# Kernel tuning notes

Measured on AMD Instinct MI355X. Metric: run time of the kernel, lower is better.

Reference implementation:

```python
import jax, jax.numpy as jnp
import numpy as np

HIDDEN = 1024
N_ROUTED = 16
N_SHARED = 2
TOP_K = 2
MID_R = HIDDEN // 4   # routed_ratio=4 -> 256
MID_S = HIDDEN // 2   # shared_ratio=2 -> 512


def setup_inputs() -> dict:
    key = jax.random.key(0)
    ks = jax.random.split(key, 8)
    s = 0.02
    return {
        "x": jax.random.normal(ks[0], (2, 1024, HIDDEN), dtype=jnp.float32),
        "router_w": jax.random.normal(ks[1], (HIDDEN, N_ROUTED), dtype=jnp.float32) * s,
        "wg_r": jax.random.normal(ks[2], (N_ROUTED, HIDDEN, MID_R), dtype=jnp.float32) * s,
        "wu_r": jax.random.normal(ks[3], (N_ROUTED, HIDDEN, MID_R), dtype=jnp.float32) * s,
        "wd_r": jax.random.normal(ks[4], (N_ROUTED, MID_R, HIDDEN), dtype=jnp.float32) * s,
        "wg_s": jax.random.normal(ks[5], (N_SHARED, HIDDEN, MID_S), dtype=jnp.float32) * s,
        "wu_s": jax.random.normal(ks[6], (N_SHARED, HIDDEN, MID_S), dtype=jnp.float32) * s,
        "wd_s": jax.random.normal(ks[7], (N_SHARED, MID_S, HIDDEN), dtype=jnp.float32) * s,
    }


def reference(x, router_w, wg_r, wu_r, wd_r, wg_s, wu_s, wd_s):
    orig_shape = x.shape
    flat = x.reshape(-1, orig_shape[-1])  # [T, D]

    # ---- shared experts: sum of always-active SwiGLU FFNs ----
    gs = jnp.einsum("td,ndm->tnm", flat, wg_s)            # [T, Ns, Ms]
    us = jnp.einsum("td,ndm->tnm", flat, wu_s)
    out = jnp.einsum("tnm,nmd->td", jax.nn.silu(gs) * us, wd_s)  # summed over n

    # ---- router: softmax -> top-k -> renormalize ----
    logits = (flat @ router_w).astype(jnp.float32)        # [T, E]
    probs = jax.nn.softmax(logits, axis=-1)
    weights, indices = jax.lax.top_k(probs, TOP_K)        # [T, K]
    weights = weights / (weights.sum(axis=-1, keepdims=True) + 1e-9)
    weights = weights.astype(x.dtype)

    # combine weights as dense [T, E] (top-k indices are distinct)
    comb = jnp.sum(jax.nn.one_hot(indices, N_ROUTED, dtype=x.dtype)
                   * weights[..., None], axis=1)          # [T, E]

    # ---- routed experts (dense dispatch; combine folded into hidden) ----
    g = jnp.einsum("td,edm->tem", flat, wg_r)             # [T, E, Mr]
    u = jnp.einsum("td,edm->tem", flat, wu_r)
    h = jax.nn.silu(g) * u                                 # [T, E, Mr]
    h = h * comb[:, :, None]                               # weight before down-proj (linear)
    out = out + jnp.einsum("tem,emd->td", h, wd_r)

    return out.reshape(orig_shape)
```

## Files before the change

kernel.cpp:

```cpp
#include <hip/hip_runtime.h>
#include <hip/hip_bf16.h>
#include <stdint.h>

#define T_TOK 2048
#define DHID  1024
#define NEXP  16
#define MR    256
#define MS    512
#define CAP   512

typedef float  f32x4  __attribute__((ext_vector_type(4)));
typedef __bf16 bf16x8 __attribute__((ext_vector_type(8)));

typedef __attribute__((address_space(3))) void       lds_void;
typedef const __attribute__((address_space(1))) void gbl_void;

#define GLOAD16(g, l) __builtin_amdgcn_global_load_lds((gbl_void*)(g), (lds_void*)(l), 16, 0, 0)
#define VMCNT8() asm volatile("s_waitcnt vmcnt(8)" ::: "memory")
#define VMCNT0() asm volatile("s_waitcnt vmcnt(0)" ::: "memory")
#define SCHED_FENCE() __builtin_amdgcn_sched_barrier(0)

__device__ __forceinline__ void barrier_raw() {
  asm volatile("" ::: "memory");
  __builtin_amdgcn_s_barrier();
  asm volatile("" ::: "memory");
}

__device__ __forceinline__ ushort f2bf(float f) {
  uint32_t u = __float_as_uint(f);
  u = (u + 0x7fffu + ((u >> 16) & 1u)) >> 16;
  return (ushort)u;
}
__device__ __forceinline__ float bf2f(ushort v) { return __uint_as_float(((uint32_t)v) << 16); }

__device__ __forceinline__ void stage128(const ushort* __restrict__ g0, int strideE,
                                         ushort* lds, int tid) {
  const int wave = tid >> 6;
  const int r = tid >> 3, colE = (tid & 7) * 8;
#pragma unroll
  for (int s = 0; s < 4; ++s) {
    const int row = s * 32 + r;
    GLOAD16(g0 + (size_t)row * strideE + (colE ^ ((row & 7) << 3)), lds + s * 2048 + wave * 512);
  }
}

__device__ __forceinline__ void stage_gather128(const ushort* __restrict__ xb,
                                                const int tok[4], int k0,
                                                ushort* lds, int tid) {
  const int wave = tid >> 6;
  const int r = tid >> 3, colE = (tid & 7) * 8;
#pragma unroll
  for (int s = 0; s < 4; ++s) {
    const int row = s * 32 + r;
    GLOAD16(xb + (size_t)tok[s] * DHID + k0 + (colE ^ ((row & 7) << 3)), lds + s * 2048 + wave * 512);
  }
}

__device__ __forceinline__ void mfma_tile(const ushort* a_sh, const ushort* b_sh,
                                          int wr, int wc, int lane, f32x4 (&acc)[4][4]) {
  const int rb = lane & 15;
  const int sw = (rb & 7) << 3;
#pragma unroll
  for (int kk = 0; kk < 64; kk += 32) {
    const int k8 = (kk + ((lane >> 4) << 3)) ^ sw;
    bf16x8 af[4];
#pragma unroll
    for (int m = 0; m < 4; m++)
      af[m] = *(const bf16x8*)&a_sh[(wr * 64 + m * 16 + rb) * 64 + k8];
#pragma unroll
    for (int n = 0; n < 4; n++) {
      bf16x8 bf = *(const bf16x8*)&b_sh[(wc * 64 + n * 16 + rb) * 64 + k8];
#pragma unroll
      for (int m = 0; m < 4; m++)
        acc[m][n] = __builtin_amdgcn_mfma_f32_16x16x32_bf16(af[m], bf, acc[m][n], 0, 0, 0);
    }
  }
}

__device__ __forceinline__ bool queue_lookup(const int* __restrict__ cnt, int mti,
                                             int& e_out, int& s0_out, int& c_out) {
  int acc = 0;
#pragma unroll
  for (int ee = 0; ee < NEXP; ++ee) {
    const int c = cnt[ee];
    const int ntl = (c + 127) >> 7;
    if (mti < acc + ntl) { e_out = ee; s0_out = (mti - acc) << 7; c_out = c; return true; }
    acc += ntl;
  }
  return false;
}

struct TP {
  const float* in; ushort* out;
  int R, C, out_ld, ilv;
  long long out_batch;
};

__device__ __forceinline__ void tpose_tile(const TP p, int local, void* smem, int tid) {
  float (*t_sh)[65] = (float(*)[65])smem;
  const int tr = p.R >> 6, tc = p.C >> 6, per = tr * tc;
  const int b = local / per, rem = local - b * per;
  const int rt = rem / tc, ct = rem - rt * tc;
  const int r0 = rt * 64, c0 = ct * 64;
  const float* ip = p.in + (size_t)b * p.R * p.C;
  ushort* op = p.out + (size_t)b * p.out_batch;
  const int trd = tid >> 4, tcd = (tid & 15) * 4;
#pragma unroll
  for (int q = 0; q < 4; q++) {
    float4 v = *(const float4*)&ip[(size_t)(r0 + trd + q * 16) * p.C + c0 + tcd];
    t_sh[trd + q * 16][tcd + 0] = v.x; t_sh[trd + q * 16][tcd + 1] = v.y;
    t_sh[trd + q * 16][tcd + 2] = v.z; t_sh[trd + q * 16][tcd + 3] = v.w;
  }
  __syncthreads();
#pragma unroll
  for (int q = 0; q < 4; q++) {
    const int cc = trd + q * 16;
    int rr = c0 + cc;
    if (p.ilv) rr = ((rr >> 4) << 5) + (rr & 15);
    ushort4 o;
    o.x = f2bf(t_sh[tcd + 0][cc]); o.y = f2bf(t_sh[tcd + 1][cc]);
    o.z = f2bf(t_sh[tcd + 2][cc]); o.w = f2bf(t_sh[tcd + 3][cc]);
    *(ushort4*)&op[(size_t)rr * p.out_ld + r0 + tcd] = o;
  }
}

__global__ __launch_bounds__(256) void k_prep(
    const float* __restrict__ x, const float* __restrict__ rw,
    ushort* __restrict__ xb, int* __restrict__ topi, float2* __restrict__ topw)
{
  __shared__ float rw_sh[NEXP][DHID];
  const int tid = threadIdx.x;
#pragma unroll
  for (int it = 0; it < 16; ++it) {
    const int flat = it * 1024 + tid * 4;
    float4 v = *(const float4*)&rw[flat];
    const int d = flat >> 4, e = flat & 15;
    rw_sh[e + 0][d] = v.x; rw_sh[e + 1][d] = v.y;
    rw_sh[e + 2][d] = v.z; rw_sh[e + 3][d] = v.w;
  }
  __syncthreads();

  const int wave = tid >> 6, lane = tid & 63;
  for (int tk = 0; tk < 2; ++tk) {
    const int t = blockIdx.x * 8 + wave * 2 + tk;
    const float* xp = x + (size_t)t * DHID;
    float acc[NEXP];
#pragma unroll
    for (int e = 0; e < NEXP; e++) acc[e] = 0.f;
#pragma unroll
    for (int i = 0; i < 4; ++i) {
      const int d4 = i * 64 + lane;
      float4 xv = *(const float4*)&xp[d4 * 4];
      ushort4 o; o.x = f2bf(xv.x); o.y = f2bf(xv.y); o.z = f2bf(xv.z); o.w = f2bf(xv.w);
      *(ushort4*)&xb[(size_t)t * DHID + d4 * 4] = o;
#pragma unroll
      for (int e = 0; e < NEXP; e++) {
        float4 wv = *(const float4*)&rw_sh[e][d4 * 4];
        acc[e] = fmaf(xv.x, wv.x, acc[e]);
        acc[e] = fmaf(xv.y, wv.y, acc[e]);
        acc[e] = fmaf(xv.z, wv.z, acc[e]);
        acc[e] = fmaf(xv.w, wv.w, acc[e]);
      }
    }
#pragma unroll
    for (int off = 32; off >= 1; off >>= 1) {
#pragma unroll
      for (int e = 0; e < NEXP; e++) acc[e] += __shfl_xor(acc[e], off, 64);
    }
    if (lane == 0) {
      float m = acc[0];
#pragma unroll
      for (int e = 1; e < NEXP; e++) m = fmaxf(m, acc[e]);
      float p[NEXP], Z = 0.f;
#pragma unroll
      for (int e = 0; e < NEXP; e++) { p[e] = __expf(acc[e] - m); Z += p[e]; }
      const float inv = 1.f / Z;
      int i1 = 0; float p1 = p[0] * inv;
      for (int e = 1; e < NEXP; e++) { float pe = p[e] * inv; if (pe > p1) { p1 = pe; i1 = e; } }
      int i2 = -1; float p2 = -1.f;
      for (int e = 0; e < NEXP; e++) { if (e == i1) continue; float pe = p[e] * inv; if (pe > p2) { p2 = pe; i2 = e; } }
      const float denom = p1 + p2 + 1e-9f;
      topi[t] = i1 | (i2 << 8);
      topw[t] = make_float2(p1 / denom, p2 / denom);
    }
  }
}

__global__ __launch_bounds__(256) void k_build_tp(
    const int* __restrict__ topi, const float2* __restrict__ topw,
    int* __restrict__ cnt, int* __restrict__ ltok, float* __restrict__ lw,
    int* __restrict__ tslot, TP t0, TP t1, TP t2, TP t3)
{
  __shared__ float t_smem[64][65];
  const int tid = threadIdx.x;
  const int bid = blockIdx.x;
  if (bid >= NEXP) {
    const int local = bid - NEXP;
    if      (local < 1024) tpose_tile(t0, local,        t_smem, tid);
    else if (local < 2048) tpose_tile(t1, local - 1024, t_smem, tid);
    else if (local < 2304) tpose_tile(t2, local - 2048, t_smem, tid);
    else                   tpose_tile(t3, local - 2304, t_smem, tid);
    return;
  }
  int* wsum = (int*)t_smem;
  const int e = bid;
  const int wave = tid >> 6, lane = tid & 63;
  const int t0i = tid * 8;

  int4 a = *(const int4*)&topi[t0i];
  int4 b = *(const int4*)&topi[t0i + 4];
  int ti[8] = {a.x, a.y, a.z, a.w, b.x, b.y, b.z, b.w};
  int match[8]; int c = 0;
#pragma unroll
  for (int k = 0; k < 8; ++k) {
    const int i1 = ti[k] & 0xff, i2 = (ti[k] >> 8) & 0xff;
    match[k] = (i1 == e) ? 1 : ((i2 == e) ? 2 : 0);
    c += (match[k] != 0);
  }
  int incl = c;
#pragma unroll
  for (int off = 1; off < 64; off <<= 1) {
    int n = __shfl_up(incl, off, 64);
    if (lane >= off) incl += n;
  }
  if (lane == 63) wsum[wave] = incl;
  __syncthreads();
  int base = incl - c;
  for (int w = 0; w < wave; ++w) base += wsum[w];
  if (tid == 0) {
    int tot = wsum[0] + wsum[1] + wsum[2] + wsum[3];
    cnt[e] = tot > CAP ? CAP : tot;
  }
#pragma unroll
  for (int k = 0; k < 8; ++k) {
    if (match[k]) {
      const int t = t0i + k;
      if (base < CAP) {
        float2 w2 = topw[t];
        ltok[e * CAP + base] = t;
        lw[e * CAP + base] = (match[k] == 1) ? w2.x : w2.y;
        tslot[t * 2 + (match[k] - 1)] = e * CAP + base;
      } else {
        tslot[t * 2 + (match[k] - 1)] = -1;
      }
      base++;
    }
  }
}

__global__ __launch_bounds__(256) void k_up(
    const ushort* __restrict__ xb, const ushort* __restrict__ wguTs,
    const ushort* __restrict__ wguTr, const int* __restrict__ cnt,
    const int* __restrict__ ltok, const float* __restrict__ lw,
    ushort* __restrict__ h_s, ushort* __restrict__ h_r, TP t4, TP t5)
{
  __shared__ ushort smem[4 * 128 * 64];
  ushort (*r_sh)[64] = (ushort(*)[64])smem;
  const int tid = threadIdx.x, lane = tid & 63, wave = tid >> 6;
  const int wr = wave >> 1, wc = wave & 1;
  const int rb = lane & 15, rowoff = (lane >> 4) << 2;
  const int bid0 = blockIdx.x;
  if (bid0 >= 512) {
    const int local = bid0 - 512;
    if (local < 1024) tpose_tile(t4, local, smem, tid);
    else              tpose_tile(t5, local - 1024, smem, tid);
    return;
  }
  f32x4 acc[4][4] = {};

  if (bid0 < 256) {
    const int bid = (bid0 & 7) * 32 + (bid0 >> 3);
    const int mt = bid & 15, nt = bid >> 4;
    const ushort* Ab = xb + (size_t)mt * 128 * DHID;
    const ushort* Bb = wguTs + (size_t)nt * 128 * DHID;
    stage128(Ab, DHID, smem, tid);
    stage128(Bb, DHID, smem + 16384, tid);
    for (int t = 0; t < 16; ++t) {
      const int co = (t & 1) * 8192;
      const int no = ((t + 1) & 1) * 8192;
      if (t < 15) {
        stage128(Ab + (t + 1) * 64, DHID, smem + no, tid);
        stage128(Bb + (t + 1) * 64, DHID, smem + 16384 + no, tid);
        SCHED_FENCE();
        VMCNT8();
      } else {
        SCHED_FENCE();
        VMCNT0();
      }
      SCHED_FENCE();
      barrier_raw();
      SCHED_FENCE();
      mfma_tile(smem + co, smem + 16384 + co, wr, wc, lane, acc);
      SCHED_FENCE();
      barrier_raw();
    }
#pragma unroll
    for (int m = 0; m < 4; m++)
#pragma unroll
      for (int p = 0; p < 2; p++) {
        f32x4 g = acc[m][2 * p], u = acc[m][2 * p + 1];
#pragma unroll
        for (int jj = 0; jj < 4; jj++) {
          float gv = g[jj];
          float hv = (gv / (1.f + __expf(-gv))) * u[jj];
          r_sh[wr * 64 + m * 16 + rowoff + jj][wc * 32 + p * 16 + rb] = f2bf(hv);
        }
      }
    __syncthreads();
#pragma unroll
    for (int sp = 0; sp < 4; sp++) {
      const int row = sp * 32 + (tid >> 3), col = (tid & 7) * 8;
      *(uint4*)&h_s[(size_t)(mt * 128 + row) * DHID + nt * 64 + col] = *(const uint4*)&r_sh[row][col];
    }
  } else {
    const int id = bid0 - 256;
    const int mti = id >> 2, ntile = id & 3;
    int e, s0, c;
    if (!queue_lookup(cnt, mti, e, s0, c)) return;
    int tok[4];
#pragma unroll
    for (int s = 0; s < 4; ++s) {
      int slot = s0 + s * 32 + (tid >> 3);
      if (slot >= c) slot = c - 1;
      tok[s] = ltok[e * CAP + slot];
    }
    const ushort* Bb = wguTr + ((size_t)e * 512 + ntile * 128) * DHID;
    stage_gather128(xb, tok, 0, smem, tid);
    stage128(Bb, DHID, smem + 16384, tid);
    for (int t = 0; t < 16; ++t) {
      const int co = (t & 1) * 8192;
      const int no = ((t + 1) & 1) * 8192;
      if (t < 15) {
        stage_gather128(xb, tok, (t + 1) * 64, smem + no, tid);
        stage128(Bb + (t + 1) * 64, DHID, smem + 16384 + no, tid);
        SCHED_FENCE();
        VMCNT8();
      } else {
        SCHED_FENCE();
        VMCNT0();
      }
      SCHED_FENCE();
      barrier_raw();
      SCHED_FENCE();
      mfma_tile(smem + co, smem + 16384 + co, wr, wc, lane, acc);
      SCHED_FENCE();
      barrier_raw();
    }
#pragma unroll
    for (int m = 0; m < 4; m++)
#pragma unroll
      for (int jj = 0; jj < 4; jj++) {
        const int slot = s0 + wr * 64 + m * 16 + rowoff + jj;
        const float w = (slot < c) ? lw[e * CAP + slot] : 0.f;
#pragma unroll
        for (int p = 0; p < 2; p++) {
          float gv = acc[m][2 * p][jj];
          float hv = (gv / (1.f + __expf(-gv))) * acc[m][2 * p + 1][jj] * w;
          r_sh[wr * 64 + m * 16 + rowoff + jj][wc * 32 + p * 16 + rb] = f2bf(hv);
        }
      }
    __syncthreads();
#pragma unroll
    for (int sp = 0; sp < 4; sp++) {
      const int row = sp * 32 + (tid >> 3), col = (tid & 7) * 8;
      *(uint4*)&h_r[((size_t)e * CAP + s0 + row) * MR + ntile * 64 + col] = *(const uint4*)&r_sh[row][col];
    }
  }
}

__global__ __launch_bounds__(256) void k_down(
    const ushort* __restrict__ h_s, const ushort* __restrict__ wdTs,
    const ushort* __restrict__ h_r, const ushort* __restrict__ wdTr,
    const int* __restrict__ cnt, ushort* __restrict__ ds, ushort* __restrict__ dr)
{
  __shared__ ushort smem[4 * 128 * 64];
  ushort (*r2)[128] = (ushort(*)[128])smem;
  const int tid = threadIdx.x, lane = tid & 63, wave = tid >> 6;
  const int wr = wave >> 1, wc = wave & 1;
  const int rb = lane & 15, rowoff = (lane >> 4) << 2;
  f32x4 acc[4][4] = {};
  const int bid0 = blockIdx.x;

  const ushort* Ab; const ushort* Bb;
  int K, rowbase, colbase; ushort* outp;
  if (bid0 < 128) {
    const int bid = (bid0 & 7) * 16 + (bid0 >> 3);
    const int mt = bid >> 3, nt = bid & 7;
    Ab = h_s + (size_t)mt * 128 * DHID;
    Bb = wdTs + (size_t)nt * 128 * DHID;
    K = DHID; rowbase = mt * 128; colbase = nt * 128;
    outp = ds;
  } else {
    const int id = bid0 - 128;
    const int mti = id >> 3, nt = id & 7;
    int e, s0, c;
    if (!queue_lookup(cnt, mti, e, s0, c)) return;
    Ab = h_r + ((size_t)e * CAP + s0) * MR;
    Bb = wdTr + ((size_t)e * DHID + nt * 128) * MR;
    K = MR; rowbase = e * CAP + s0; colbase = nt * 128;
    outp = dr;
  }
  const int nk = K >> 6;
  stage128(Ab, K, smem, tid);
  stage128(Bb, K, smem + 16384, tid);
  for (int t = 0; t < nk; ++t) {
    const int co = (t & 1) * 8192;
    const int no = ((t + 1) & 1) * 8192;
    if (t + 1 < nk) {
      stage128(Ab + (t + 1) * 64, K, smem + no, tid);
      stage128(Bb + (t + 1) * 64, K, smem + 16384 + no, tid);
      SCHED_FENCE();
      VMCNT8();
    } else {
      SCHED_FENCE();
      VMCNT0();
    }
    SCHED_FENCE();
    barrier_raw();
    SCHED_FENCE();
    mfma_tile(smem + co, smem + 16384 + co, wr, wc, lane, acc);
    SCHED_FENCE();
    barrier_raw();
  }
#pragma unroll
  for (int m = 0; m < 4; m++)
#pragma unroll
    for (int n = 0; n < 4; n++) {
      f32x4 v = acc[m][n];
#pragma unroll
      for (int jj = 0; jj < 4; jj++)
        r2[wr * 64 + m * 16 + rowoff + jj][wc * 64 + n * 16 + rb] = f2bf(v[jj]);
    }
  __syncthreads();
  {
    const int row = tid >> 1, colE = (tid & 1) * 64;
    ushort* op = &outp[(size_t)(rowbase + row) * DHID + colbase + colE];
#pragma unroll
    for (int q = 0; q < 8; q++)
      *(uint4*)(op + q * 8) = *(const uint4*)&r2[row][colE + q * 8];
  }
}

__global__ __launch_bounds__(256) void k_comb(
    const ushort* __restrict__ ds, const ushort* __restrict__ dr,
    const int* __restrict__ tslot, float* __restrict__ out)
{
  const int tid = threadIdx.x;
  const int t = blockIdx.x * 2 + (tid >> 7);
  const int d = (tid & 127) * 8;
  const int es1 = tslot[t * 2], es2 = tslot[t * 2 + 1];
  uint4 a = *(const uint4*)&ds[(size_t)t * DHID + d];
  float r[8];
  const ushort* ap = (const ushort*)&a;
#pragma unroll
  for (int k = 0; k < 8; ++k) r[k] = bf2f(ap[k]);
  if (es1 >= 0) {
    uint4 b = *(const uint4*)&dr[(size_t)es1 * DHID + d];
    const ushort* bp = (const ushort*)&b;
#pragma unroll
    for (int k = 0; k < 8; ++k) r[k] += bf2f(bp[k]);
  }
  if (es2 >= 0) {
    uint4 b = *(const uint4*)&dr[(size_t)es2 * DHID + d];
    const ushort* bp = (const ushort*)&b;
#pragma unroll
    for (int k = 0; k < 8; ++k) r[k] += bf2f(bp[k]);
  }
  float4* op = (float4*)&out[(size_t)t * DHID + d];
  op[0] = make_float4(r[0], r[1], r[2], r[3]);
  op[1] = make_float4(r[4], r[5], r[6], r[7]);
}

extern "C" void kernel_launch(void* const* d_in, const int* in_sizes, int n_in,
                              void* d_out, int out_size, void* d_ws, size_t ws_size,
                              hipStream_t stream) {
  const float* x    = (const float*)d_in[0];
  const float* rw   = (const float*)d_in[1];
  const float* wg_r = (const float*)d_in[2];
  const float* wu_r = (const float*)d_in[3];
  const float* wd_r = (const float*)d_in[4];
  const float* wg_s = (const float*)d_in[5];
  const float* wu_s = (const float*)d_in[6];
  const float* wd_s = (const float*)d_in[7];
  float* out = (float*)d_out;

  char* ws = (char*)d_ws;
  size_t off = 0;
  ushort* xb    = (ushort*)(ws + off); off += (size_t)T_TOK * DHID * 2;
  ushort* wguTs = (ushort*)(ws + off); off += (size_t)2048 * DHID * 2;
  ushort* wdTs  = (ushort*)(ws + off); off += (size_t)DHID * DHID * 2;
  ushort* wguTr = (ushort*)(ws + off); off += (size_t)NEXP * 512 * DHID * 2;
  ushort* wdTr  = (ushort*)(ws + off); off += (size_t)NEXP * DHID * MR * 2;
  ushort* h_s   = (ushort*)(ws + off); off += (size_t)T_TOK * DHID * 2;
  ushort* h_r   = (ushort*)(ws + off); off += (size_t)NEXP * CAP * MR * 2;
  ushort* ds    = (ushort*)(ws + off); off += (size_t)T_TOK * DHID * 2;
  ushort* dr    = (ushort*)(ws + off); off += (size_t)NEXP * CAP * DHID * 2;
  int*    cnt   = (int*)(ws + off);    off += 256;
  int*    ltok  = (int*)(ws + off);    off += (size_t)NEXP * CAP * 4;
  float*  lw    = (float*)(ws + off);  off += (size_t)NEXP * CAP * 4;
  int*    topi  = (int*)(ws + off);    off += (size_t)T_TOK * 4;
  float2* topw  = (float2*)(ws + off); off += (size_t)T_TOK * 8;
  int*    tslot = (int*)(ws + off);    off += (size_t)T_TOK * 2 * 4;
  if (off > ws_size) return;

  TP t0 = {wg_r, wguTr,             DHID, MR,   DHID, 1, (long long)512 * DHID};
  TP t1 = {wu_r, wguTr + 16 * DHID, DHID, MR,   DHID, 1, (long long)512 * DHID};
  TP t2 = {wg_s, wguTs,             DHID, MS,   DHID, 1, (long long)1024 * DHID};
  TP t3 = {wu_s, wguTs + 16 * DHID, DHID, MS,   DHID, 1, (long long)1024 * DHID};
  TP t4 = {wd_r, wdTr,              MR,   DHID, MR,   0, (long long)DHID * MR};
  TP t5 = {wd_s, wdTs,              MS,   DHID, DHID, 0, (long long)MS};

  k_prep<<<T_TOK / 8, 256, 0, stream>>>(x, rw, xb, topi, topw);
  k_build_tp<<<NEXP + 2560, 256, 0, stream>>>(topi, topw, cnt, ltok, lw, tslot, t0, t1, t2, t3);
  k_up<<<512 + 1280, 256, 0, stream>>>(xb, wguTs, wguTr, cnt, ltok, lw, h_s, h_r, t4, t5);
  k_down<<<640, 256, 0, stream>>>(h_s, wdTs, h_r, wdTr, cnt, ds, dr);
  k_comb<<<T_TOK / 2, 256, 0, stream>>>(ds, dr, tslot, out);
}
```

Measured before the change: 75.99 us.

## Triple-buffer B operand to prefetch weights two K-steps ahead

```diff
diff --git a/kernel.cpp b/kernel.cpp
--- a/kernel.cpp
+++ b/kernel.cpp
@@ -16,9 +16,13 @@
 typedef const __attribute__((address_space(1))) void gbl_void;
 
 #define GLOAD16(g, l) __builtin_amdgcn_global_load_lds((gbl_void*)(g), (lds_void*)(l), 16, 0, 0)
-#define VMCNT8() asm volatile("s_waitcnt vmcnt(8)" ::: "memory")
-#define VMCNT0() asm volatile("s_waitcnt vmcnt(0)" ::: "memory")
+#define VMCNT12() asm volatile("s_waitcnt vmcnt(12)" ::: "memory")
+#define VMCNT8()  asm volatile("s_waitcnt vmcnt(8)" ::: "memory")
+#define VMCNT0()  asm volatile("s_waitcnt vmcnt(0)" ::: "memory")
 #define SCHED_FENCE() __builtin_amdgcn_sched_barrier(0)
+
+#define AOFF(t) (((t) & 1) * 8192)
+#define BOFF(t) (16384 + ((t) % 3) * 8192)
 
 __device__ __forceinline__ void barrier_raw() {
   asm volatile("" ::: "memory");
@@ -254,7 +258,7 @@
     const int* __restrict__ ltok, const float* __restrict__ lw,
     ushort* __restrict__ h_s, ushort* __restrict__ h_r, TP t4, TP t5)
 {
-  __shared__ ushort smem[4 * 128 * 64];
+  __shared__ ushort smem[5 * 128 * 64];
   ushort (*r_sh)[64] = (ushort(*)[64])smem;
   const int tid = threadIdx.x, lane = tid & 63, wave = tid >> 6;
   const int wr = wave >> 1, wc = wave & 1;
@@ -273,24 +277,19 @@
     const int mt = bid & 15, nt = bid >> 4;
     const ushort* Ab = xb + (size_t)mt * 128 * DHID;
     const ushort* Bb = wguTs + (size_t)nt * 128 * DHID;
-    stage128(Ab, DHID, smem, tid);
-    stage128(Bb, DHID, smem + 16384, tid);
+    stage128(Bb, DHID, smem + BOFF(0), tid);
+    stage128(Ab, DHID, smem + AOFF(0), tid);
+    stage128(Bb + 64, DHID, smem + BOFF(1), tid);
     for (int t = 0; t < 16; ++t) {
-      const int co = (t & 1) * 8192;
-      const int no = ((t + 1) & 1) * 8192;
-      if (t < 15) {
-        stage128(Ab + (t + 1) * 64, DHID, smem + no, tid);
-        stage128(Bb + (t + 1) * 64, DHID, smem + 16384 + no, tid);
-        SCHED_FENCE();
-        VMCNT8();
-      } else {
-        SCHED_FENCE();
-        VMCNT0();
-      }
+      if (t + 1 < 16) stage128(Ab + (t + 1) * 64, DHID, smem + AOFF(t + 1), tid);
+      if (t + 2 < 16) stage128(Bb + (t + 2) * 64, DHID, smem + BOFF(t + 2), tid);
+      SCHED_FENCE();
+      const int rem = 15 - t;
+      if (rem >= 2) { VMCNT12(); } else if (rem == 1) { VMCNT8(); } else { VMCNT0(); }
       SCHED_FENCE();
       barrier_raw();
       SCHED_FENCE();
-      mfma_tile(smem + co, smem + 16384 + co, wr, wc, lane, acc);
+      mfma_tile(smem + AOFF(t), smem + BOFF(t), wr, wc, lane, acc);
       SCHED_FENCE();
       barrier_raw();
     }
@@ -325,24 +324,19 @@
       tok[s] = ltok[e * CAP + slot];
     }
     const ushort* Bb = wguTr + ((size_t)e * 512 + ntile * 128) * DHID;
-    stage_gather128(xb, tok, 0, smem, tid);
-    stage128(Bb, DHID, smem + 16384, tid);
+    stage128(Bb, DHID, smem + BOFF(0), tid);
+    stage_gather128(xb, tok, 0, smem + AOFF(0), tid);
+    stage128(Bb + 64, DHID, smem + BOFF(1), tid);
     for (int t = 0; t < 16; ++t) {
-      const int co = (t & 1) * 8192;
-      const int no = ((t + 1) & 1) * 8192;
-      if (t < 15) {
-        stage_gather128(xb, tok, (t + 1) * 64, smem + no, tid);
-        stage128(Bb + (t + 1) * 64, DHID, smem + 16384 + no, tid);
-        SCHED_FENCE();
-        VMCNT8();
-      } else {
-        SCHED_FENCE();
-        VMCNT0();
-      }
+      if (t + 1 < 16) stage_gather128(xb, tok, (t + 1) * 64, smem + AOFF(t + 1), tid);
+      if (t + 2 < 16) stage128(Bb + (t + 2) * 64, DHID, smem + BOFF(t + 2), tid);
+      SCHED_FENCE();
+      const int rem = 15 - t;
+      if (rem >= 2) { VMCNT12(); } else if (rem == 1) { VMCNT8(); } else { VMCNT0(); }
       SCHED_FENCE();
       barrier_raw();
       SCHED_FENCE();
-      mfma_tile(smem + co, smem + 16384 + co, wr, wc, lane, acc);
+      mfma_tile(smem + AOFF(t), smem + BOFF(t), wr, wc, lane, acc);
       SCHED_FENCE();
       barrier_raw();
     }
@@ -373,7 +367,7 @@
     const ushort* __restrict__ h_r, const ushort* __restrict__ wdTr,
     const int* __restrict__ cnt, ushort* __restrict__ ds, ushort* __restrict__ dr)
 {
-  __shared__ ushort smem[4 * 128 * 64];
+  __shared__ ushort smem[5 * 128 * 64];
   ushort (*r2)[128] = (ushort(*)[128])smem;
   const int tid = threadIdx.x, lane = tid & 63, wave = tid >> 6;
   const int wr = wave >> 1, wc = wave & 1;
@@ -401,24 +395,19 @@
     outp = dr;
   }
   const int nk = K >> 6;
-  stage128(Ab, K, smem, tid);
-  stage128(Bb, K, smem + 16384, tid);
+  stage128(Bb, K, smem + BOFF(0), tid);
+  stage128(Ab, K, smem + AOFF(0), tid);
+  stage128(Bb + 64, K, smem + BOFF(1), tid);
   for (int t = 0; t < nk; ++t) {
-    const int co = (t & 1) * 8192;
-    const int no = ((t + 1) & 1) * 8192;
-    if (t + 1 < nk) {
-      stage128(Ab + (t + 1) * 64, K, smem + no, tid);
-      stage128(Bb + (t + 1) * 64, K, smem + 16384 + no, tid);
-      SCHED_FENCE();
-      VMCNT8();
-    } else {
-      SCHED_FENCE();
-      VMCNT0();
-    }
+    if (t + 1 < nk) stage128(Ab + (t + 1) * 64, K, smem + AOFF(t + 1), tid);
+    if (t + 2 < nk) stage128(Bb + (t + 2) * 64, K, smem + BOFF(t + 2), tid);
+    SCHED_FENCE();
+    const int rem = nk - 1 - t;
+    if (rem >= 2) { VMCNT12(); } else if (rem == 1) { VMCNT8(); } else { VMCNT0(); }
     SCHED_FENCE();
     barrier_raw();
     SCHED_FENCE();
-    mfma_tile(smem + co, smem + 16384 + co, wr, wc, lane, acc);
+    mfma_tile(smem + AOFF(t), smem + BOFF(t), wr, wc, lane, acc);
     SCHED_FENCE();
     barrier_raw();
   }
```

New measurement: 77.41 us. About the same (+1.9%).
